# Optimization experiments

Measured on AMD Instinct MI355X. Metric: run time of the kernel, lower is better.

Reference implementation:

```python
import jax, jax.numpy as jnp
import numpy as np

B, C, H, W = 16, 256, 32, 32
K = 3          # kernel size
KK = K * K     # matrix_batch = 9 kernel positions
N = 256        # out_channels = n (power of 2, nstack = 1)


def setup_inputs() -> dict:
    key = jax.random.key(0)
    k1, k2, k3, k4 = jax.random.split(key, 4)
    s = 1.0 / np.sqrt(2.0)  # repo's 'regular' param init scale
    return {
        "x": jax.random.normal(k1, (B, C, H, W), jnp.float32),
        "twiddle1": jax.random.normal(k2, (KK, N - 1, 2, 2), jnp.float32) * s,
        "twiddle2": jax.random.normal(k3, (KK, N - 1, 2, 2), jnp.float32) * s,
        "bias": jax.random.normal(k4, (KK, N), jnp.float32) * 0.01,
    }


def _butterfly_tied(twiddle, x, increasing):
    """Tied-weight butterfly multiply.
    twiddle: (s, n-1, 2, 2); x: (b, s, n). At stride st, twiddle[:, st-1:2*st-1]
    (length st) is shared across the n/(2*st) blocks (matches butterfly_mult_torch).
    """
    b, s, n = x.shape
    m = n.bit_length() - 1  # log2(n)
    strides = [1 << i for i in range(m)]
    if not increasing:
        strides = strides[::-1]
    for st in strides:
        t = twiddle[:, st - 1:2 * st - 1]            # (s, st, 2, 2)
        xr = x.reshape(b, s, n // (2 * st), 2, st)   # (b, s, g, 2, st)
        # out[b,s,g,i,l] = sum_k t[s,l,i,k] * xr[b,s,g,k,l]
        x = jnp.einsum('slik,bsgkl->bsgil', t, xr).reshape(b, s, n)
    return x


def reference(x, twiddle1, twiddle2, bias):
    b, c, h, w = x.shape
    # im2col / F.unfold with kernel 3, pad 1, stride 1 -> (b, c, 9, h*w),
    # kernel positions in row-major order (matches torch unfold layout).
    xp = jnp.pad(x, ((0, 0), (0, 0), (1, 1), (1, 1)))
    patches = jnp.stack(
        [xp[:, :, i:i + h, j:j + w] for i in range(K) for j in range(K)], axis=2
    )  # (b, c, 9, h, w)
    inp = patches.reshape(b, c, KK, h * w).transpose(0, 3, 2, 1)
    inp = inp.reshape(b * h * w, KK, c)  # (batch*h*w, 9, c)
    # BB^T: B^T (decreasing stride) then B (increasing stride), bias on last.
    y = _butterfly_tied(twiddle1, inp, increasing=False)
    y = _butterfly_tied(twiddle2, y, increasing=True) + bias  # bias: (9, N)
    out = y.mean(axis=1)  # average over the 9 kernel positions -> (b*h*w, N)
    return out.reshape(b, h * w, N).transpose(0, 2, 1).reshape(b, N, h, w)
```

## Files before the change

### kernel.cpp

```cpp
#include <hip/hip_runtime.h>
#include <hip/hip_bf16.h>

typedef __attribute__((ext_vector_type(8))) short short8;
typedef __attribute__((ext_vector_type(4))) float float4v;
typedef __attribute__((ext_vector_type(16))) float float16v;

#define XT_BYTES (16*32*34*34*8*2)
#define WG_BYTES (9*4*4*8*64*8*2)

__global__ __launch_bounds__(256) void k_prep(const float* __restrict__ x,
                                              const float* __restrict__ tw1,
                                              const float* __restrict__ tw2,
                                              const float* __restrict__ bias,
                                              __hip_bfloat16* __restrict__ xTg,
                                              __hip_bfloat16* __restrict__ Wg,
                                              float* __restrict__ biasout) {
  __shared__ __align__(16) char smem[256 * 33 * 4];
  int blk = blockIdx.x;
  int tid = threadIdx.x;

  if (blk < 512) {
    float* tile = (float*)smem;
    char* xTB = (char*)xTg;
    int h = blk & 31, b = blk >> 5;
    {
      int w4 = (tid & 7) * 4, c0 = tid >> 3;
#pragma unroll
      for (int j = 0; j < 8; ++j) {
        int ci = c0 + 32 * j;
        float4 v = *(const float4*)&x[((b * 256 + ci) * 32 + h) * 32 + w4];
        *(float4*)&tile[ci * 33 + w4] = v;
      }
    }
    __syncthreads();
    {
      int g0 = tid >> 5, w = tid & 31;
#pragma unroll
      for (int gi = 0; gi < 4; ++gi) {
        int g = gi * 8 + g0;
        union { short8 s; __hip_bfloat16 hv[8]; } pk;
#pragma unroll
        for (int cc = 0; cc < 8; ++cc)
          pk.hv[cc] = __float2bfloat16(tile[(g * 8 + cc) * 33 + w]);
        *(short8*)(xTB + ((((b * 32 + g) * 34 + h + 1) * 34) + (w + 1)) * 16) = pk.s;
      }
    }
    if (h < 2) {
      uint4 z4 = {0u, 0u, 0u, 0u};
      int edge = h * 33;
      for (int i = tid; i < 32 * 34; i += 256) {
        int g = i / 34, w = i - g * 34;
        *(uint4*)(xTB + ((((b * 32 + g) * 34 + edge) * 34) + w) * 16) = z4;
      }
      for (int i = tid; i < 32 * 32; i += 256) {
        int g = i >> 5, hh = 1 + (i & 31);
        *(uint4*)(xTB + ((((b * 32 + g) * 34 + hh) * 34) + edge) * 16) = z4;
      }
    }
    return;
  }

  int wblk = blk - 512;
  if (wblk == 144) {
    if (tid < 256) {
      float a = 0.f;
#pragma unroll
      for (int s = 0; s < 9; ++s) a += bias[s * 256 + tid];
      biasout[tid] = a * (1.f / 9.f);
    }
    return;
  }
  float* mat = (float*)smem;
  float* tws = (float*)(smem + 17408);
  int sidx = wblk >> 4;
  int colbase = (wblk & 15) * 16;

  for (int i = tid; i < 255 * 4; i += 256) {
    tws[i]           = tw1[sidx * 255 * 4 + i];
    tws[255 * 4 + i] = tw2[sidx * 255 * 4 + i];
  }
  {
    int r = tid;
#pragma unroll
    for (int c = 0; c < 16; ++c) mat[r * 17 + c] = (r == colbase + c) ? 1.f : 0.f;
  }

  int c  = tid & 15;
  int pg = tid >> 4;
  for (int ph = 0; ph < 2; ++ph) {
    for (int si = 0; si < 8; ++si) {
      int lg = ph ? si : (7 - si);
      int st = 1 << lg;
      __syncthreads();
      float x0[8], x1[8], t0[8], t1[8], t2[8], t3[8];
#pragma unroll
      for (int i = 0; i < 8; ++i) {
        int qp = pg * 8 + i;
        int li = qp & (st - 1);
        int gi = qp >> lg;
        int p0 = (gi << (lg + 1)) | li;
        int p1 = p0 + st;
        float4 tv = *(const float4*)&tws[(ph * 255 + st - 1 + li) * 4];
        t0[i] = tv.x; t1[i] = tv.y; t2[i] = tv.z; t3[i] = tv.w;
        x0[i] = mat[p0 * 17 + c];
        x1[i] = mat[p1 * 17 + c];
      }
#pragma unroll
      for (int i = 0; i < 8; ++i) {
        int qp = pg * 8 + i;
        int li = qp & (st - 1);
        int gi = qp >> lg;
        int p0 = (gi << (lg + 1)) | li;
        int p1 = p0 + st;
        mat[p0 * 17 + c] = t0[i] * x0[i] + t1[i] * x1[i];
        mat[p1 * 17 + c] = t2[i] * x0[i] + t3[i] * x1[i];
      }
    }
  }
  __syncthreads();

  for (int idx = tid; idx < 256 * 16; idx += 256) {
    int r = idx >> 4, cc = idx & 15;
    int cg = colbase + cc;
    int pr = cg >> 6, g = (cg >> 3) & 7, c8 = cg & 7;
    int nq = r >> 6, nl = r & 63;
    int o = ((((sidx * 4 + pr) * 4 + nq) * 8 + g) * 64 + nl) * 8 + c8;
    Wg[o] = __float2bfloat16(mat[r * 17 + cc] * (1.f / 9.f));
  }
}

__global__ __launch_bounds__(256, 4) void k_gemm(const __hip_bfloat16* __restrict__ xTg,
                                                 const __hip_bfloat16* __restrict__ Wg,
                                                 const float* __restrict__ biasout,
                                                 float* __restrict__ out) {
  __shared__ __align__(64) char lds[32768];
  const char* WgB = (const char*)Wg;
  const char* xTB = (const char*)xTg;

  int blk  = blockIdx.x;
  int rest = blk >> 3;
  int b    = 2 * (blk & 7) + (rest >> 6);
  int r2   = rest & 63;
  int nq   = r2 & 3;
  int pt   = r2 >> 2;
  int h0   = pt * 2;

  int tid  = threadIdx.x;
  int lane = tid & 63;
  int wk   = tid >> 6;
  int half = lane >> 5;
  int l31  = lane & 31;

  float16v acc[2][2];
#pragma unroll
  for (int mt = 0; mt < 2; ++mt)
#pragma unroll
    for (int p2 = 0; p2 < 2; ++p2)
#pragma unroll
      for (int e = 0; e < 16; ++e) acc[mt][p2][e] = 0.f;

  int aoff = ((2 * wk + half) * 64 + l31) * 16;
  int bbase = ((((b * 32 + 2 * wk + half) * 34 + h0) * 34) + l31) * 16;

#pragma unroll 2
  for (int p = 0; p < 4; ++p) {
    const char* Bp = xTB + bbase + p * (8 * 34 * 34) * 16;
    const char* Ap = WgB + (p * 4 + nq) * 8192;
#pragma unroll
    for (int si = 0; si < 3; ++si) {
#pragma unroll
      for (int sj = 0; sj < 3; ++sj) {
        const char* Aslab = Ap + (si * 3 + sj) * (16 * 8192);
        short8 a0 = *(const short8*)(Aslab + aoff);
        short8 a1 = *(const short8*)(Aslab + aoff + 32 * 16);
        const char* Bq = Bp + (si * 34 + sj) * 16;
        short8 b0 = *(const short8*)(Bq);
        short8 b1 = *(const short8*)(Bq + 34 * 16);
        acc[0][0] = __builtin_amdgcn_mfma_f32_32x32x16_bf16(a0, b0, acc[0][0], 0, 0, 0);
        acc[0][1] = __builtin_amdgcn_mfma_f32_32x32x16_bf16(a0, b1, acc[0][1], 0, 0, 0);
        acc[1][0] = __builtin_amdgcn_mfma_f32_32x32x16_bf16(a1, b0, acc[1][0], 0, 0, 0);
        acc[1][1] = __builtin_amdgcn_mfma_f32_32x32x16_bf16(a1, b1, acc[1][1], 0, 0, 0);
      }
    }
  }

  float bv[16];
  if (wk < 2) {
#pragma unroll
    for (int reg = 0; reg < 16; ++reg)
      bv[reg] = biasout[nq * 64 + wk * 32 + (reg & 3) + 8 * (reg >> 2) + 4 * half];
  }

  auto st16 = [&](int slot, const float16v& v) {
    char* base = lds + slot * 4096 + lane * 16;
    *(float4v*)(base)        = (float4v){v[0],  v[1],  v[2],  v[3]};
    *(float4v*)(base + 1024) = (float4v){v[4],  v[5],  v[6],  v[7]};
    *(float4v*)(base + 2048) = (float4v){v[8],  v[9],  v[10], v[11]};
    *(float4v*)(base + 3072) = (float4v){v[12], v[13], v[14], v[15]};
  };
  auto ld16add = [&](int slot, float16v& v) {
    const char* base = lds + slot * 4096 + lane * 16;
    float4v t0 = *(const float4v*)(base);
    float4v t1 = *(const float4v*)(base + 1024);
    float4v t2 = *(const float4v*)(base + 2048);
    float4v t3 = *(const float4v*)(base + 3072);
    v[0] += t0[0]; v[1] += t0[1]; v[2]  += t0[2]; v[3]  += t0[3];
    v[4] += t1[0]; v[5] += t1[1]; v[6]  += t1[2]; v[7]  += t1[3];
    v[8] += t2[0]; v[9] += t2[1]; v[10] += t2[2]; v[11] += t2[3];
    v[12] += t3[0]; v[13] += t3[1]; v[14] += t3[2]; v[15] += t3[3];
  };

  __syncthreads();
  if (wk == 2) { st16(0, acc[0][0]); st16(1, acc[0][1]); st16(2, acc[1][0]); st16(3, acc[1][1]); }
  if (wk == 3) { st16(4, acc[0][0]); st16(5, acc[0][1]); st16(6, acc[1][0]); st16(7, acc[1][1]); }
  __syncthreads();
  if (wk == 0) { ld16add(0, acc[0][0]); ld16add(1, acc[0][1]); ld16add(2, acc[1][0]); ld16add(3, acc[1][1]); }
  if (wk == 1) { ld16add(4, acc[0][0]); ld16add(5, acc[0][1]); ld16add(6, acc[1][0]); ld16add(7, acc[1][1]); }
  __syncthreads();
  if (wk == 1) { st16(0, acc[0][0]); st16(1, acc[0][1]); }
  if (wk == 0) { st16(4, acc[1][0]); st16(5, acc[1][1]); }
  __syncthreads();
  if (wk == 0) {
    ld16add(0, acc[0][0]); ld16add(1, acc[0][1]);
#pragma unroll
    for (int reg = 0; reg < 16; ++reg) {
      int n = nq * 64 + (reg & 3) + 8 * (reg >> 2) + 4 * half;
      float* o0 = &out[((b * 256 + n) * 32 + h0) * 32 + l31];
      o0[0]  = acc[0][0][reg] + bv[reg];
      o0[32] = acc[0][1][reg] + bv[reg];
    }
  }
  if (wk == 1) {
    ld16add(4, acc[1][0]); ld16add(5, acc[1][1]);
#pragma unroll
    for (int reg = 0; reg < 16; ++reg) {
      int n = nq * 64 + 32 + (reg & 3) + 8 * (reg >> 2) + 4 * half;
      float* o0 = &out[((b * 256 + n) * 32 + h0) * 32 + l31];
      o0[0]  = acc[1][0][reg] + bv[reg];
      o0[32] = acc[1][1][reg] + bv[reg];
    }
  }
}

extern "C" void kernel_launch(void* const* d_in, const int* in_sizes, int n_in,
                              void* d_out, int out_size, void* d_ws, size_t ws_size,
                              hipStream_t stream) {
  const float* x    = (const float*)d_in[0];
  const float* tw1  = (const float*)d_in[1];
  const float* tw2  = (const float*)d_in[2];
  const float* bias = (const float*)d_in[3];
  float* out = (float*)d_out;

  char* ws = (char*)d_ws;
  __hip_bfloat16* xTg = (__hip_bfloat16*)ws;
  __hip_bfloat16* Wg  = (__hip_bfloat16*)(ws + XT_BYTES);
  float* biasout      = (float*)(ws + XT_BYTES + WG_BYTES);

  k_prep<<<657, 256, 0, stream>>>(x, tw1, tw2, bias, xTg, Wg, biasout);
  k_gemm<<<1024, 256, 0, stream>>>(xTg, Wg, biasout, out);
}
```

Before: 107.8 us.

## Stage im2col input tile in LDS and split output channels across waves

The GEMM kernel now uses 512-thread blocks, one per (batch, row pair), covering all 256 output channels. Each of the 8 waves owns a 32-channel slice and accumulates over the full reduction. The shifted input tile for each 16-group stage is staged into LDS once and shared by all waves. This replaces per-wave global loads plus the cross-wave LDS reduction epilogue. It cuts redundant global input reads and the reduction syncs, but the grid shrinks to 256 blocks, which may underfill the GPU, and each stage adds syncs around the LDS fill.

```diff
diff --git a/kernel.cpp b/kernel.cpp
--- a/kernel.cpp
+++ b/kernel.cpp
@@ -2,7 +2,6 @@
 #include <hip/hip_bf16.h>
 
 typedef __attribute__((ext_vector_type(8))) short short8;
-typedef __attribute__((ext_vector_type(4))) float float4v;
 typedef __attribute__((ext_vector_type(16))) float float16v;
 
 #define XT_BYTES (16*32*34*34*8*2)
@@ -129,116 +128,75 @@
   }
 }
 
-__global__ __launch_bounds__(256, 4) void k_gemm(const __hip_bfloat16* __restrict__ xTg,
+__global__ __launch_bounds__(512, 2) void k_gemm(const __hip_bfloat16* __restrict__ xTg,
                                                  const __hip_bfloat16* __restrict__ Wg,
                                                  const float* __restrict__ biasout,
                                                  float* __restrict__ out) {
-  __shared__ __align__(64) char lds[32768];
+  __shared__ __align__(128) char lds[34816];
   const char* WgB = (const char*)Wg;
   const char* xTB = (const char*)xTg;
 
   int blk  = blockIdx.x;
   int rest = blk >> 3;
-  int b    = 2 * (blk & 7) + (rest >> 6);
-  int r2   = rest & 63;
-  int nq   = r2 & 3;
-  int pt   = r2 >> 2;
+  int b    = 2 * (blk & 7) + (rest >> 4);
+  int pt   = rest & 15;
   int h0   = pt * 2;
 
-  int tid  = threadIdx.x;
-  int lane = tid & 63;
-  int wk   = tid >> 6;
-  int half = lane >> 5;
-  int l31  = lane & 31;
-
-  float16v acc[2][2];
-#pragma unroll
-  for (int mt = 0; mt < 2; ++mt)
-#pragma unroll
-    for (int p2 = 0; p2 < 2; ++p2)
-#pragma unroll
-      for (int e = 0; e < 16; ++e) acc[mt][p2][e] = 0.f;
-
-  int aoff = ((2 * wk + half) * 64 + l31) * 16;
-  int bbase = ((((b * 32 + 2 * wk + half) * 34 + h0) * 34) + l31) * 16;
-
-#pragma unroll 2
-  for (int p = 0; p < 4; ++p) {
-    const char* Bp = xTB + bbase + p * (8 * 34 * 34) * 16;
-    const char* Ap = WgB + (p * 4 + nq) * 8192;
+  int tid   = threadIdx.x;
+  int lane  = tid & 63;
+  int w8    = tid >> 6;
+  int nq    = w8 >> 1;
+  int nhalf = w8 & 1;
+  int half  = lane >> 5;
+  int l31   = lane & 31;
+
+  float16v acc[2];
+#pragma unroll
+  for (int p2 = 0; p2 < 2; ++p2)
+#pragma unroll
+    for (int e = 0; e < 16; ++e) acc[p2][e] = 0.f;
+
+  const char* pA = WgB + nq * 8192 + (nhalf * 32 + l31) * 16;
+
+#pragma unroll 1
+  for (int st = 0; st < 2; ++st) {
+    __syncthreads();
+    for (int c = tid; c < 2176; c += 512) {
+      int g   = c / 136;
+      int rem = c - g * 136;
+      int r   = rem / 34;
+      int col = rem - r * 34;
+      short8 v = *(const short8*)(xTB + (b * 32 + st * 16 + g) * 18496 +
+                                  (h0 + r) * 544 + col * 16);
+      *(short8*)(lds + c * 16) = v;
+    }
+    __syncthreads();
 #pragma unroll
     for (int si = 0; si < 3; ++si) {
 #pragma unroll
       for (int sj = 0; sj < 3; ++sj) {
-        const char* Aslab = Ap + (si * 3 + sj) * (16 * 8192);
-        short8 a0 = *(const short8*)(Aslab + aoff);
-        short8 a1 = *(const short8*)(Aslab + aoff + 32 * 16);
-        const char* Bq = Bp + (si * 34 + sj) * 16;
-        short8 b0 = *(const short8*)(Bq);
-        short8 b1 = *(const short8*)(Bq + 34 * 16);
-        acc[0][0] = __builtin_amdgcn_mfma_f32_32x32x16_bf16(a0, b0, acc[0][0], 0, 0, 0);
-        acc[0][1] = __builtin_amdgcn_mfma_f32_32x32x16_bf16(a0, b1, acc[0][1], 0, 0, 0);
-        acc[1][0] = __builtin_amdgcn_mfma_f32_32x32x16_bf16(a1, b0, acc[1][0], 0, 0, 0);
-        acc[1][1] = __builtin_amdgcn_mfma_f32_32x32x16_bf16(a1, b1, acc[1][1], 0, 0, 0);
-      }
-    }
-  }
-
-  float bv[16];
-  if (wk < 2) {
-#pragma unroll
-    for (int reg = 0; reg < 16; ++reg)
-      bv[reg] = biasout[nq * 64 + wk * 32 + (reg & 3) + 8 * (reg >> 2) + 4 * half];
-  }
-
-  auto st16 = [&](int slot, const float16v& v) {
-    char* base = lds + slot * 4096 + lane * 16;
-    *(float4v*)(base)        = (float4v){v[0],  v[1],  v[2],  v[3]};
-    *(float4v*)(base + 1024) = (float4v){v[4],  v[5],  v[6],  v[7]};
-    *(float4v*)(base + 2048) = (float4v){v[8],  v[9],  v[10], v[11]};
-    *(float4v*)(base + 3072) = (float4v){v[12], v[13], v[14], v[15]};
-  };
-  auto ld16add = [&](int slot, float16v& v) {
-    const char* base = lds + slot * 4096 + lane * 16;
-    float4v t0 = *(const float4v*)(base);
-    float4v t1 = *(const float4v*)(base + 1024);
-    float4v t2 = *(const float4v*)(base + 2048);
-    float4v t3 = *(const float4v*)(base + 3072);
-    v[0] += t0[0]; v[1] += t0[1]; v[2]  += t0[2]; v[3]  += t0[3];
-    v[4] += t1[0]; v[5] += t1[1]; v[6]  += t1[2]; v[7]  += t1[3];
-    v[8] += t2[0]; v[9] += t2[1]; v[10] += t2[2]; v[11] += t2[3];
-    v[12] += t3[0]; v[13] += t3[1]; v[14] += t3[2]; v[15] += t3[3];
-  };
-
-  __syncthreads();
-  if (wk == 2) { st16(0, acc[0][0]); st16(1, acc[0][1]); st16(2, acc[1][0]); st16(3, acc[1][1]); }
-  if (wk == 3) { st16(4, acc[0][0]); st16(5, acc[0][1]); st16(6, acc[1][0]); st16(7, acc[1][1]); }
-  __syncthreads();
-  if (wk == 0) { ld16add(0, acc[0][0]); ld16add(1, acc[0][1]); ld16add(2, acc[1][0]); ld16add(3, acc[1][1]); }
-  if (wk == 1) { ld16add(4, acc[0][0]); ld16add(5, acc[0][1]); ld16add(6, acc[1][0]); ld16add(7, acc[1][1]); }
-  __syncthreads();
-  if (wk == 1) { st16(0, acc[0][0]); st16(1, acc[0][1]); }
-  if (wk == 0) { st16(4, acc[1][0]); st16(5, acc[1][1]); }
-  __syncthreads();
-  if (wk == 0) {
-    ld16add(0, acc[0][0]); ld16add(1, acc[0][1]);
-#pragma unroll
-    for (int reg = 0; reg < 16; ++reg) {
-      int n = nq * 64 + (reg & 3) + 8 * (reg >> 2) + 4 * half;
-      float* o0 = &out[((b * 256 + n) * 32 + h0) * 32 + l31];
-      o0[0]  = acc[0][0][reg] + bv[reg];
-      o0[32] = acc[0][1][reg] + bv[reg];
-    }
-  }
-  if (wk == 1) {
-    ld16add(4, acc[1][0]); ld16add(5, acc[1][1]);
-#pragma unroll
-    for (int reg = 0; reg < 16; ++reg) {
-      int n = nq * 64 + 32 + (reg & 3) + 8 * (reg >> 2) + 4 * half;
-      float* o0 = &out[((b * 256 + n) * 32 + h0) * 32 + l31];
-      o0[0]  = acc[1][0][reg] + bv[reg];
-      o0[32] = acc[1][1][reg] + bv[reg];
-    }
+#pragma unroll
+        for (int t = 0; t < 8; ++t) {
+          const short8 a = *(const short8*)(pA +
+              (si * 3 + sj) * 131072 + (st * 2 + (t >> 2)) * 32768 +
+              ((2 * t + half) & 7) * 1024);
+          const char* bb = lds + (((2 * t + half) * 4 + si) * 34 + sj + l31) * 16;
+          short8 b0 = *(const short8*)(bb);
+          short8 b1 = *(const short8*)(bb + 544);
+          acc[0] = __builtin_amdgcn_mfma_f32_32x32x16_bf16(a, b0, acc[0], 0, 0, 0);
+          acc[1] = __builtin_amdgcn_mfma_f32_32x32x16_bf16(a, b1, acc[1], 0, 0, 0);
+        }
+      }
+    }
+  }
+
+#pragma unroll
+  for (int reg = 0; reg < 16; ++reg) {
+    int n = nq * 64 + nhalf * 32 + (reg & 3) + 8 * (reg >> 2) + 4 * half;
+    float bv = biasout[n];
+    float* o0 = &out[((b * 256 + n) * 32 + h0) * 32 + l31];
+    o0[0]  = acc[0][reg] + bv;
+    o0[32] = acc[1][reg] + bv;
   }
 }
 
@@ -257,5 +215,5 @@
   float* biasout      = (float*)(ws + XT_BYTES + WG_BYTES);
 
   k_prep<<<657, 256, 0, stream>>>(x, tw1, tw2, bias, xTg, Wg, biasout);
-  k_gemm<<<1024, 256, 0, stream>>>(xTg, Wg, biasout, out);
+  k_gemm<<<256, 512, 0, stream>>>(xTg, Wg, biasout, out);
 }
```

Result: slower. 116.9 us (+8.5%).

## Compute butterfly weight matrix in registers with wave shuffles instead of LDS

Applied to the files above, without the earlier changes.

The weight-building blocks of the prep kernel used to run 16 butterfly stages over a 256x16 matrix in shared memory, with a block barrier between stages. Each thread now holds 16 consecutive rows of one column in registers. Small strides are done inside the thread and large strides via __shfl_xor within the 64-lane wavefront, which removes the LDS traffic and the 16 barriers. Only the prep kernel's weight path changes and the GEMM is untouched, so the overall effect is likely small.

```diff
diff --git a/kernel.cpp b/kernel.cpp
--- a/kernel.cpp
+++ b/kernel.cpp
@@ -70,8 +70,7 @@
     }
     return;
   }
-  float* mat = (float*)smem;
-  float* tws = (float*)(smem + 17408);
+  float* tws = (float*)smem;
   int sidx = wblk >> 4;
   int colbase = (wblk & 15) * 16;
 
@@ -79,54 +78,58 @@
     tws[i]           = tw1[sidx * 255 * 4 + i];
     tws[255 * 4 + i] = tw2[sidx * 255 * 4 + i];
   }
+  __syncthreads();
+
+  int c  = tid >> 4;
+  int rg = tid & 15;
+  int cg = colbase + c;
+
+  float xr[16];
+#pragma unroll
+  for (int j = 0; j < 16; ++j) xr[j] = (rg * 16 + j == cg) ? 1.f : 0.f;
+
+#define RSTAGE(PH, ST)                                                        \
+  {                                                                           \
+    _Pragma("unroll")                                                         \
+    for (int base = 0; base < 16; base += 2 * (ST)) {                         \
+      _Pragma("unroll")                                                       \
+      for (int q = 0; q < (ST); ++q) {                                        \
+        float4 tv = *(const float4*)&tws[((PH) * 255 + (ST) - 1 + q) * 4];    \
+        float x0 = xr[base + q], x1 = xr[base + q + (ST)];                    \
+        xr[base + q]        = tv.x * x0 + tv.y * x1;                          \
+        xr[base + q + (ST)] = tv.z * x0 + tv.w * x1;                          \
+      }                                                                       \
+    }                                                                         \
+  }
+
+#define SSTAGE(PH, ST, M)                                                     \
+  {                                                                           \
+    int lib = (rg & ((M) - 1)) * 16;                                          \
+    bool lower = (rg & (M)) == 0;                                             \
+    _Pragma("unroll")                                                         \
+    for (int j = 0; j < 16; ++j) {                                            \
+      float y = __shfl_xor(xr[j], (M), 64);                                   \
+      float4 tv = *(const float4*)&tws[((PH) * 255 + (ST) - 1 + lib + j) * 4];\
+      xr[j] = lower ? (tv.x * xr[j] + tv.y * y)                               \
+                    : (tv.z * y + tv.w * xr[j]);                              \
+    }                                                                         \
+  }
+
+  SSTAGE(0, 128, 8) SSTAGE(0, 64, 4) SSTAGE(0, 32, 2) SSTAGE(0, 16, 1)
+  RSTAGE(0, 8) RSTAGE(0, 4) RSTAGE(0, 2) RSTAGE(0, 1)
+  RSTAGE(1, 1) RSTAGE(1, 2) RSTAGE(1, 4) RSTAGE(1, 8)
+  SSTAGE(1, 16, 1) SSTAGE(1, 32, 2) SSTAGE(1, 64, 4) SSTAGE(1, 128, 8)
+
   {
-    int r = tid;
-#pragma unroll
-    for (int c = 0; c < 16; ++c) mat[r * 17 + c] = (r == colbase + c) ? 1.f : 0.f;
-  }
-
-  int c  = tid & 15;
-  int pg = tid >> 4;
-  for (int ph = 0; ph < 2; ++ph) {
-    for (int si = 0; si < 8; ++si) {
-      int lg = ph ? si : (7 - si);
-      int st = 1 << lg;
-      __syncthreads();
-      float x0[8], x1[8], t0[8], t1[8], t2[8], t3[8];
-#pragma unroll
-      for (int i = 0; i < 8; ++i) {
-        int qp = pg * 8 + i;
-        int li = qp & (st - 1);
-        int gi = qp >> lg;
-        int p0 = (gi << (lg + 1)) | li;
-        int p1 = p0 + st;
-        float4 tv = *(const float4*)&tws[(ph * 255 + st - 1 + li) * 4];
-        t0[i] = tv.x; t1[i] = tv.y; t2[i] = tv.z; t3[i] = tv.w;
-        x0[i] = mat[p0 * 17 + c];
-        x1[i] = mat[p1 * 17 + c];
-      }
-#pragma unroll
-      for (int i = 0; i < 8; ++i) {
-        int qp = pg * 8 + i;
-        int li = qp & (st - 1);
-        int gi = qp >> lg;
-        int p0 = (gi << (lg + 1)) | li;
-        int p1 = p0 + st;
-        mat[p0 * 17 + c] = t0[i] * x0[i] + t1[i] * x1[i];
-        mat[p1 * 17 + c] = t2[i] * x0[i] + t3[i] * x1[i];
-      }
-    }
-  }
-  __syncthreads();
-
-  for (int idx = tid; idx < 256 * 16; idx += 256) {
-    int r = idx >> 4, cc = idx & 15;
-    int cg = colbase + cc;
     int pr = cg >> 6, g = (cg >> 3) & 7, c8 = cg & 7;
-    int nq = r >> 6, nl = r & 63;
-    int o = ((((sidx * 4 + pr) * 4 + nq) * 8 + g) * 64 + nl) * 8 + c8;
-    Wg[o] = __float2bfloat16(mat[r * 17 + cc] * (1.f / 9.f));
-  }
+    int nq = rg >> 2;
+    int o0 = ((((sidx * 4 + pr) * 4 + nq) * 8 + g) * 64 + (rg & 3) * 16) * 8 + c8;
+#pragma unroll
+    for (int j = 0; j < 16; ++j)
+      Wg[o0 + j * 8] = __float2bfloat16(xr[j] * (1.f / 9.f));
+  }
+#undef RSTAGE
+#undef SSTAGE
 }
 
 __global__ __launch_bounds__(256, 4) void k_gemm(const __hip_bfloat16* __restrict__ xTg,
```

Result: slower. 112.9 us (+4.7%).
